# Kernel tuning notes

Measured on AMD Instinct MI355X. Metric: run time of the kernel, lower is better.

Reference implementation:

```python
import jax, jax.numpy as jnp
import numpy as np

TEMP = 0.2
EPS = 1e-12  # F.normalize eps


def setup_inputs() -> dict:
    key = jax.random.key(0)
    k1, k2 = jax.random.split(key)
    l, B, K, D = 4, 64, 32, 128
    emb_i = jax.random.normal(k1, (l, B, K, D), dtype=jnp.float32)
    emb_j = jax.random.normal(k2, (l, B, K, D), dtype=jnp.float32)
    joint_valid = jnp.ones((B, K), dtype=jnp.float32)
    return {"emb_i": emb_i, "emb_j": emb_j, "joint_valid": joint_valid}


def _l2norm(x):
    n = jnp.sqrt(jnp.sum(x * x, axis=-1, keepdims=True))
    return x / jnp.maximum(n, EPS)


def reference(emb_i, emb_j, joint_valid):
    l, B, K, D = emb_i.shape
    N = B * K
    z_i = _l2norm(emb_i.reshape(l, N, D))
    z_j = _l2norm(emb_j.reshape(l, N, D))
    reps = jnp.concatenate([z_i, z_j], axis=1)              # (l, 2N, D), unit rows
    # cosine similarity of unit vectors == matmul
    sim = jnp.einsum('lnd,lmd->lnm', reps, reps)            # (l, 2N, 2N)
    idx = jnp.arange(N)
    pos = sim[:, idx, idx + N]                              # diag offset +N, (l, N)
    # note: original code uses the SAME +N offset diagonal for both ij and ji
    positives = jnp.concatenate([pos, pos], axis=1)         # (l, 2N)
    neg_mask = 1.0 - jnp.eye(2 * N, dtype=sim.dtype)        # (2N, 2N)
    denom = jnp.sum(neg_mask[None] * jnp.exp(sim / TEMP), axis=2)  # (l, 2N)
    loss_partial = -jnp.log(jnp.exp(positives / TEMP) / denom)    # (l, 2N)
    joints_mask = joint_valid.reshape(1, 1, B, K)
    all_num = jnp.sum(joint_valid)
    loss = jnp.sum(loss_partial.reshape(l, 2, B, K) * joints_mask) / (2.0 * all_num)
    return loss
```

## Files before the change

kernel.cpp:

```cpp
#include <hip/hip_runtime.h>
#include <hip/hip_bf16.h>

typedef __attribute__((ext_vector_type(8))) short short8;
typedef __attribute__((ext_vector_type(4))) float floatx4;

#define NROWS 4096
#define NHALF 2048
#define DDIM  128
#define LDST  136
#define SQRT_SCALE 2.6857914f
#define LN2 0.69314718056f

#define WS_ROWSUM_OFF 64
#define WS_DIAG_OFF   16448
#define WS_POS_OFF    32832
#define WS_Z_BYTE_OFF 196864

__device__ inline unsigned short f2bf(float f) {
    unsigned u = __builtin_bit_cast(unsigned, f);
    u += 0x7fffu + ((u >> 16) & 1u);
    return (unsigned short)(u >> 16);
}

__global__ __launch_bounds__(256) void k_norm(const float* __restrict__ emb_i,
                                              const float* __restrict__ emb_j,
                                              const float* __restrict__ jv,
                                              float* __restrict__ wsf,
                                              unsigned short* __restrict__ z) {
    int bx = blockIdx.x, tid = threadIdx.x;
    if (bx == 4096) {
        __shared__ float sred[256];
        float s = 0.f;
        #pragma unroll
        for (int i = 0; i < 8; ++i) s += jv[tid + 256 * i];
        sred[tid] = s; __syncthreads();
        for (int off = 128; off > 0; off >>= 1) {
            if (tid < off) sred[tid] += sred[tid + off];
            __syncthreads();
        }
        if (tid == 0) wsf[1] = sred[0];
        return;
    }
    int gid = bx * 256 + tid;
    if (gid == 0) { wsf[0] = 0.f; *(unsigned*)&wsf[2] = 0u; }
    if (gid >= WS_ROWSUM_OFF && gid < WS_ROWSUM_OFF + 16384) wsf[gid] = 0.f;

    int wave = tid >> 6, lane = tid & 63;
    int r = bx * 4 + wave;
    int l = r >> 12, n = r & 4095;
    const float* src = (n < NHALF) ? (emb_i + ((size_t)l * NHALF + n) * DDIM)
                                   : (emb_j + ((size_t)l * NHALF + (n - NHALF)) * DDIM);
    float2 v = *(const float2*)(src + lane * 2);
    float ss = v.x * v.x + v.y * v.y;
    #pragma unroll
    for (int off = 1; off < 64; off <<= 1) ss += __shfl_xor(ss, off);
    float inv = SQRT_SCALE / fmaxf(sqrtf(ss), 1e-12f);
    unsigned pack = ((unsigned)f2bf(v.y * inv) << 16) | (unsigned)f2bf(v.x * inv);
    *(unsigned*)(z + (size_t)r * DDIM + lane * 2) = pack;
}

__global__ __launch_bounds__(256) void k_sim(const unsigned short* __restrict__ z,
                                             float* __restrict__ rowsum,
                                             float* __restrict__ diag,
                                             float* __restrict__ pos) {
    __shared__ __align__(16) unsigned short lds[128 * LDST];
    int bx = blockIdx.x, tid = threadIdx.x;
    int l = bx & 3, idx = bx >> 2;
    int J = (int)((sqrtf(8.f * (float)idx + 1.f) - 1.f) * 0.5f);
    while ((J + 1) * (J + 2) / 2 <= idx) ++J;
    while (J * (J + 1) / 2 > idx) --J;
    int I = idx - J * (J + 1) / 2;
    int wave = tid >> 6, lane = tid & 63, m = lane & 15, quad = lane >> 4;
    const unsigned short* zl = z + (size_t)l * NROWS * DDIM;
    int l4 = l * NROWS;
    int wr0 = I * 128 + wave * 32;
    int cg0 = J * 128;

    short8 a[2][4];
    #pragma unroll
    for (int rs = 0; rs < 2; ++rs) {
        const unsigned short* p = zl + (size_t)(wr0 + rs * 16 + m) * DDIM + quad * 8;
        #pragma unroll
        for (int kk = 0; kk < 4; ++kk) a[rs][kk] = *(const short8*)(p + kk * 32);
    }
    floatx4 rsum[2];
    #pragma unroll
    for (int rs = 0; rs < 2; ++rs) rsum[rs] = (floatx4){0.f, 0.f, 0.f, 0.f};
    float csum[8];
    #pragma unroll
    for (int g = 0; g < 8; ++g) csum[g] = 0.f;

    #pragma unroll
    for (int i = 0; i < 8; ++i) {
        int chunk = tid + 256 * i;
        int col = chunk >> 4, off = chunk & 15;
        uint4 d = *(const uint4*)(zl + (size_t)(cg0 + col) * DDIM + off * 8);
        *(uint4*)&lds[col * LDST + off * 8] = d;
    }
    __syncthreads();

    #pragma unroll
    for (int cs = 0; cs < 8; ++cs) {
        int ct = cg0 + cs * 16;
        const unsigned short* lp = &lds[(cs * 16 + m) * LDST + quad * 8];
        short8 b0 = *(const short8*)(lp);
        short8 b1 = *(const short8*)(lp + 32);
        short8 b2 = *(const short8*)(lp + 64);
        short8 b3 = *(const short8*)(lp + 96);
        #pragma unroll
        for (int rs = 0; rs < 2; ++rs) {
            floatx4 acc = (floatx4){0.f, 0.f, 0.f, 0.f};
            acc = __builtin_amdgcn_mfma_f32_16x16x32_bf16(a[rs][0], b0, acc, 0, 0, 0);
            acc = __builtin_amdgcn_mfma_f32_16x16x32_bf16(a[rs][1], b1, acc, 0, 0, 0);
            acc = __builtin_amdgcn_mfma_f32_16x16x32_bf16(a[rs][2], b2, acc, 0, 0, 0);
            acc = __builtin_amdgcn_mfma_f32_16x16x32_bf16(a[rs][3], b3, acc, 0, 0, 0);
            int rowbase = wr0 + rs * 16;
            bool isdiag = (ct == rowbase);
            bool ispos  = (ct == rowbase + 2048);
            if (isdiag || ispos) {
                int c = m - (quad << 2);
                if (c >= 0 && c < 4) {
                    float v = acc[c];
                    if (isdiag) diag[l4 + rowbase + m] = v;
                    else {
                        pos[l4 + rowbase + m] = v;
                        pos[l4 + rowbase + m + NHALF] = v;
                    }
                }
            }
            float t = 0.f;
            #pragma unroll
            for (int c = 0; c < 4; ++c) {
                float e = __builtin_amdgcn_exp2f(acc[c]);
                rsum[rs][c] += e;
                t += e;
            }
            csum[cs] += t;
        }
    }
    #pragma unroll
    for (int off = 1; off < 16; off <<= 1)
        #pragma unroll
        for (int rs = 0; rs < 2; ++rs)
            #pragma unroll
            for (int c = 0; c < 4; ++c)
                rsum[rs][c] += __shfl_xor(rsum[rs][c], off);
    if (m == 0) {
        #pragma unroll
        for (int rs = 0; rs < 2; ++rs)
            #pragma unroll
            for (int c = 0; c < 4; ++c) {
                int rg = wr0 + rs * 16 + quad * 4 + c;
                atomicAdd(&rowsum[l4 + rg], rsum[rs][c]);
            }
    }
    if (I != J) {
        __syncthreads();
        float* cred = (float*)lds;
        #pragma unroll
        for (int g = 0; g < 8; ++g) {
            float v = csum[g];
            v += __shfl_xor(v, 16);
            v += __shfl_xor(v, 32);
            if (quad == 0) cred[wave * 128 + g * 16 + m] = v;
        }
        __syncthreads();
        if (tid < 128) {
            float s = cred[tid] + cred[tid + 128] + cred[tid + 256] + cred[tid + 384];
            atomicAdd(&rowsum[l4 + cg0 + tid], s);
        }
    }
}

__global__ __launch_bounds__(256) void k_loss(const float* __restrict__ jv,
                                              const float* __restrict__ rowsum,
                                              const float* __restrict__ diag,
                                              const float* __restrict__ pos,
                                              float* __restrict__ wsf,
                                              float* __restrict__ out) {
    __shared__ float sred[256];
    int tid = threadIdx.x;
    int r = blockIdx.x * 256 + tid;
    int n = r & 4095;
    float denom = rowsum[r] - __builtin_amdgcn_exp2f(diag[r]);
    float contrib = LN2 * (__builtin_amdgcn_logf(denom) - pos[r]);
    float local = contrib * jv[n & (NHALF - 1)];
    sred[tid] = local; __syncthreads();
    for (int off = 128; off > 0; off >>= 1) {
        if (tid < off) sred[tid] += sred[tid + off];
        __syncthreads();
    }
    if (tid == 0) {
        atomicAdd(&wsf[0], sred[0]);
        __threadfence();
        unsigned c = atomicAdd((unsigned*)&wsf[2], 1u);
        if (c == 63) {
            float tot = atomicAdd(&wsf[0], 0.f);
            out[0] = tot / (2.f * wsf[1]);
        }
    }
}

extern "C" void kernel_launch(void* const* d_in, const int* in_sizes, int n_in,
                              void* d_out, int out_size, void* d_ws, size_t ws_size,
                              hipStream_t stream) {
    const float* emb_i = (const float*)d_in[0];
    const float* emb_j = (const float*)d_in[1];
    const float* jv    = (const float*)d_in[2];
    float* wsf    = (float*)d_ws;
    float* rowsum = wsf + WS_ROWSUM_OFF;
    float* diag   = wsf + WS_DIAG_OFF;
    float* pos    = wsf + WS_POS_OFF;
    unsigned short* z = (unsigned short*)((char*)d_ws + WS_Z_BYTE_OFF);
    float* out = (float*)d_out;

    k_norm <<<4097, 256, 0, stream>>>(emb_i, emb_j, jv, wsf, z);
    k_sim  <<<2112, 256, 0, stream>>>(z, rowsum, diag, pos);
    k_loss <<<64,   256, 0, stream>>>(jv, rowsum, diag, pos, wsf, out);
}
```

Measured before the change: 88.29 us.

## Replace rowsum atomics with per-tile partial buffers reduced in loss kernel

Each similarity tile now writes its row and column exp-sums into a dedicated partial slot indexed by the opposite tile coordinate, instead of doing atomicAdd into a shared rowsum array. The loss kernel sums the 32 partial slots per row, and the normalize kernel no longer has to zero the rowsum buffer. This removes global atomic contention and makes the sum deterministic. In exchange the workspace grows to about 2MB of partials, and the 64-block loss kernel must read 32 times more data with little parallelism.

```diff
diff --git a/kernel.cpp b/kernel.cpp
--- a/kernel.cpp
+++ b/kernel.cpp
@@ -11,10 +11,10 @@
 #define SQRT_SCALE 2.6857914f
 #define LN2 0.69314718056f
 
-#define WS_ROWSUM_OFF 64
-#define WS_DIAG_OFF   16448
-#define WS_POS_OFF    32832
-#define WS_Z_BYTE_OFF 196864
+#define WS_PART_OFF 64
+#define WS_DIAG_OFF 524352
+#define WS_POS_OFF  540736
+#define WS_Z_BYTE_OFF 2228480
 
 __device__ inline unsigned short f2bf(float f) {
     unsigned u = __builtin_bit_cast(unsigned, f);
@@ -41,9 +41,7 @@
         if (tid == 0) wsf[1] = sred[0];
         return;
     }
-    int gid = bx * 256 + tid;
-    if (gid == 0) { wsf[0] = 0.f; *(unsigned*)&wsf[2] = 0u; }
-    if (gid >= WS_ROWSUM_OFF && gid < WS_ROWSUM_OFF + 16384) wsf[gid] = 0.f;
+    if (bx == 0 && tid == 0) { wsf[0] = 0.f; *(unsigned*)&wsf[2] = 0u; }
 
     int wave = tid >> 6, lane = tid & 63;
     int r = bx * 4 + wave;
@@ -60,7 +58,7 @@
 }
 
 __global__ __launch_bounds__(256) void k_sim(const unsigned short* __restrict__ z,
-                                             float* __restrict__ rowsum,
+                                             float* __restrict__ part,
                                              float* __restrict__ diag,
                                              float* __restrict__ pos) {
     __shared__ __align__(16) unsigned short lds[128 * LDST];
@@ -145,14 +143,13 @@
             #pragma unroll
             for (int c = 0; c < 4; ++c)
                 rsum[rs][c] += __shfl_xor(rsum[rs][c], off);
+    float* plJ = part + (size_t)(l * 32 + J) * 4096;
     if (m == 0) {
         #pragma unroll
         for (int rs = 0; rs < 2; ++rs)
             #pragma unroll
-            for (int c = 0; c < 4; ++c) {
-                int rg = wr0 + rs * 16 + quad * 4 + c;
-                atomicAdd(&rowsum[l4 + rg], rsum[rs][c]);
-            }
+            for (int c = 0; c < 4; ++c)
+                plJ[wr0 + rs * 16 + quad * 4 + c] = rsum[rs][c];
     }
     if (I != J) {
         __syncthreads();
@@ -167,13 +164,13 @@
         __syncthreads();
         if (tid < 128) {
             float s = cred[tid] + cred[tid + 128] + cred[tid + 256] + cred[tid + 384];
-            atomicAdd(&rowsum[l4 + cg0 + tid], s);
+            part[(size_t)(l * 32 + I) * 4096 + cg0 + tid] = s;
         }
     }
 }
 
 __global__ __launch_bounds__(256) void k_loss(const float* __restrict__ jv,
-                                              const float* __restrict__ rowsum,
+                                              const float* __restrict__ part,
                                               const float* __restrict__ diag,
                                               const float* __restrict__ pos,
                                               float* __restrict__ wsf,
@@ -181,8 +178,12 @@
     __shared__ float sred[256];
     int tid = threadIdx.x;
     int r = blockIdx.x * 256 + tid;
-    int n = r & 4095;
-    float denom = rowsum[r] - __builtin_amdgcn_exp2f(diag[r]);
+    int l = r >> 12, n = r & 4095;
+    const float* pl = part + (size_t)l * 32 * 4096 + n;
+    float s = 0.f;
+    #pragma unroll
+    for (int k = 0; k < 32; ++k) s += pl[(size_t)k * 4096];
+    float denom = s - __builtin_amdgcn_exp2f(diag[r]);
     float contrib = LN2 * (__builtin_amdgcn_logf(denom) - pos[r]);
     float local = contrib * jv[n & (NHALF - 1)];
     sred[tid] = local; __syncthreads();
@@ -207,14 +208,14 @@
     const float* emb_i = (const float*)d_in[0];
     const float* emb_j = (const float*)d_in[1];
     const float* jv    = (const float*)d_in[2];
-    float* wsf    = (float*)d_ws;
-    float* rowsum = wsf + WS_ROWSUM_OFF;
-    float* diag   = wsf + WS_DIAG_OFF;
-    float* pos    = wsf + WS_POS_OFF;
+    float* wsf  = (float*)d_ws;
+    float* part = wsf + WS_PART_OFF;
+    float* diag = wsf + WS_DIAG_OFF;
+    float* pos  = wsf + WS_POS_OFF;
     unsigned short* z = (unsigned short*)((char*)d_ws + WS_Z_BYTE_OFF);
     float* out = (float*)d_out;
 
     k_norm <<<4097, 256, 0, stream>>>(emb_i, emb_j, jv, wsf, z);
-    k_sim  <<<2112, 256, 0, stream>>>(z, rowsum, diag, pos);
-    k_loss <<<64,   256, 0, stream>>>(jv, rowsum, diag, pos, wsf, out);
-}
+    k_sim  <<<2112, 256, 0, stream>>>(z, part, diag, pos);
+    k_loss <<<64,   256, 0, stream>>>(jv, part, diag, pos, wsf, out);
+}
```

Result: no change. 89.27 us (+1.1%).
